# Performance work log

Hardware: AMD Instinct MI355X
Metric: run time of the kernel (lower is better)

Reference implementation:

```python
import jax, jax.numpy as jnp
import numpy as np

KERNEL = 3          # route_nms_kernel
MAX_ROUTES = 256    # max_routes (topk per image)
STRIDE = 4.0        # route_stride
MIN_SIZE = 32.0     # route_min_size
MAX_SIZE = 512.0    # route_max_size
POWER = 2.0         # route_score_power
B, H, W = 32, 512, 512


def setup_inputs() -> dict:
    key = jax.random.key(0)
    k1, k2, k3 = jax.random.split(key, 3)
    return {
        "route_logits": jax.random.normal(k1, (B, 1, H, W), dtype=jnp.float32),
        "scale_logits": jax.random.normal(k2, (B, 1, H, W), dtype=jnp.float32),
        "uncertainty_logits": jax.random.normal(k3, (B, 1, H, W), dtype=jnp.float32),
        "image_h": 2048,
        "image_w": 2048,
    }


def _local_max_pool(x):
    # x: [H, W]; 3x3 max pool, stride 1, pad kernel//2 (torch F.max_pool2d pads with -inf)
    pad = KERNEL // 2
    return jax.lax.reduce_window(x, -jnp.inf, jax.lax.max,
                                 (KERNEL, KERNEL), (1, 1),
                                 [(pad, pad), (pad, pad)])


def reference(route_logits, scale_logits, uncertainty_logits, image_h, image_w):
    # score_map = sigmoid(logits)^power * (1 - 0.35*sigmoid(uncertainty))  (use_route_uncertainty=True)
    score_map = jnp.power(jax.nn.sigmoid(route_logits), POWER)
    score_map = score_map * (1.0 - 0.35 * jax.nn.sigmoid(uncertainty_logits))
    img_h = jnp.float32(image_h)
    img_w = jnp.float32(image_w)
    width = route_logits.shape[-1]

    def per_image(batch_idx, scores2d, scale2d, unc2d):
        pooled = _local_max_pool(scores2d)
        filtered = jnp.where(scores2d == pooled, scores2d, -1.0)  # masked_fill(~mask, -1)
        values, indices = jax.lax.top_k(filtered.reshape(-1), MAX_ROUTES)
        valid = values > 0.0  # torch filters values>0; here kept as fixed-shape mask
        ys = indices // width
        xs = indices % width
        cx = (xs.astype(jnp.float32) + 0.5) * STRIDE
        cy = (ys.astype(jnp.float32) + 0.5) * STRIDE
        scale_g = scale2d[ys, xs]
        unc = jax.nn.sigmoid(unc2d[ys, xs])
        side = MIN_SIZE + jax.nn.sigmoid(scale_g) * (MAX_SIZE - MIN_SIZE)
        side = side * (1.0 + 0.25 * unc)
        half = side * 0.5
        x1 = jnp.clip(cx - half, 0.0, img_w - 1.0)
        y1 = jnp.clip(cy - half, 0.0, img_h - 1.0)
        x2 = jnp.clip(cx + half, 1.0, img_w)
        y2 = jnp.clip(cy + half, 1.0, img_h)
        rois = jnp.stack([jnp.full_like(x1, batch_idx), x1, y1, x2, y2], axis=1)  # [K,5]
        rois = jnp.where(valid[:, None], rois, 0.0)
        vals = jnp.where(valid, values, 0.0)
        return rois, vals, valid

    batch_ids = jnp.arange(route_logits.shape[0], dtype=jnp.float32)
    rois, scores, valid = jax.vmap(per_image)(
        batch_ids, score_map[:, 0], scale_logits[:, 0], uncertainty_logits[:, 0])
    # rois: [B, K, 5], scores: [B, K], valid: [B, K] (per_image_counts = valid.sum(-1))
    return rois, scores, valid
```

## Files before the change

### kernel.cpp

```cpp
#include <hip/hip_runtime.h>
#include <cstdint>
#include <cstddef>

#define BATCH 32
#define IMH 512
#define IMW 512
#define KMAX 256

#define RPW 8
#define NBLKX 2
#define NLIST (NBLKX * (IMH / RPW))
#define NMID 32
#define WCAP 512

#define TPB2 512

typedef unsigned long long u64;

__device__ __forceinline__ float sigmoidf_(float x) {
    return 1.0f / (1.0f + expf(-x));
}
__device__ __forceinline__ float scoref_(float r, float u) {
    const float sg = sigmoidf_(r);
    return sg * sg * (1.0f - 0.35f * sigmoidf_(u));
}

#define SHF(v, jj, dm) do {                                         \
    const u64 o_ = __shfl_xor((v), (jj), 64);                       \
    const bool take_ = ((((lane & (jj)) == 0) == (dm)) == ((v) < o_)); \
    (v) = take_ ? o_ : (v);                                         \
} while (0)

#define RMAX(a, b) do {                                             \
    const u64 hi_ = ((a) > (b)) ? (a) : (b);                        \
    const u64 lo_ = ((a) > (b)) ? (b) : (a);                        \
    (a) = hi_; (b) = lo_;                                           \
} while (0)

#define RMIN(a, b) do {                                             \
    const u64 hi_ = ((a) > (b)) ? (a) : (b);                        \
    const u64 lo_ = ((a) > (b)) ? (b) : (a);                        \
    (a) = lo_; (b) = hi_;                                           \
} while (0)

__device__ __forceinline__ void clean256(u64& v0, u64& v1, u64& v2, u64& v3,
                                         const int lane) {
    RMAX(v0, v2); RMAX(v1, v3);
    RMAX(v0, v1); RMAX(v2, v3);
    #pragma unroll
    for (int j = 32; j > 0; j >>= 1) {
        SHF(v0, j, true); SHF(v1, j, true); SHF(v2, j, true); SHF(v3, j, true);
    }
}

__device__ __forceinline__ void sort256(u64& v0, u64& v1, u64& v2, u64& v3,
                                        const int lane) {
    #pragma unroll
    for (int k = 2; k <= 32; k <<= 1) {
        #pragma unroll
        for (int j = k >> 1; j > 0; j >>= 1) {
            const bool dm = ((lane & k) == 0);
            SHF(v0, j, dm); SHF(v1, j, dm); SHF(v2, j, dm); SHF(v3, j, dm);
        }
    }
    #pragma unroll
    for (int j = 32; j > 0; j >>= 1) {
        SHF(v0, j, true); SHF(v1, j, false); SHF(v2, j, true); SHF(v3, j, false);
    }
    RMAX(v0, v1); RMIN(v2, v3);
    #pragma unroll
    for (int j = 32; j > 0; j >>= 1) {
        SHF(v0, j, true); SHF(v1, j, true); SHF(v2, j, false); SHF(v3, j, false);
    }
    clean256(v0, v1, v2, v3, lane);
}

__device__ __forceinline__ void merge256(u64& v0, u64& v1, u64& v2, u64& v3,
                                         u64 w0, u64 w1, u64 w2, u64 w3,
                                         const int lane) {
    const int rl = 63 ^ lane;
    const u64 b0 = __shfl(w3, rl, 64);
    const u64 b1 = __shfl(w2, rl, 64);
    const u64 b2 = __shfl(w1, rl, 64);
    const u64 b3 = __shfl(w0, rl, 64);
    v0 = (v0 > b0) ? v0 : b0;
    v1 = (v1 > b1) ? v1 : b1;
    v2 = (v2 > b2) ? v2 : b2;
    v3 = (v3 > b3) ? v3 : b3;
    clean256(v0, v1, v2, v3, lane);
}

__global__ __launch_bounds__(64)
void score_nms_kernel(const float* __restrict__ route,
                      const float* __restrict__ unc,
                      u64* __restrict__ top) {
    const int b    = blockIdx.z;
    const int lane = threadIdx.x;
    const int y0   = blockIdx.y * RPW;
    const int x0   = blockIdx.x * 256 + lane * 4;
    const int blk  = blockIdx.y * NBLKX + blockIdx.x;

    __shared__ u64 myR[WCAP];

    const float* rB = route + (size_t)b * IMH * IMW;
    const float* uB = unc   + (size_t)b * IMH * IMW;

    int ex = -1;
    if (lane == 0)       ex = x0 - 1;
    else if (lane == 63) ex = x0 + 4;
    const bool eAct = (ex >= 0 && ex < IMW);

    const u64 laneMaskLt = (1ull << lane) - 1ull;
    int wcnt = 0;

    float sP[4], hP1[4], hP2[4];
    #pragma unroll
    for (int j = 0; j < 4; ++j) { sP[j] = -INFINITY; hP1[j] = -INFINITY; hP2[j] = -INFINITY; }

    const int ylast = y0 + RPW;
    bool v = (y0 - 1 >= 0);
    float4 r4, u4; float er = 0.f, eu = 0.f;
    if (v) {
        r4 = *(const float4*)(rB + (size_t)(y0 - 1) * IMW + x0);
        u4 = *(const float4*)(uB + (size_t)(y0 - 1) * IMW + x0);
        if (eAct) { er = rB[(size_t)(y0 - 1) * IMW + ex]; eu = uB[(size_t)(y0 - 1) * IMW + ex]; }
    }

    for (int y = y0 - 1; y <= ylast; ++y) {
        const int yn = y + 1;
        const bool vn = (yn <= ylast) && (yn < IMH);
        float4 r4n, u4n; float ern = 0.f, eun = 0.f;
        if (vn) {
            r4n = *(const float4*)(rB + (size_t)yn * IMW + x0);
            u4n = *(const float4*)(uB + (size_t)yn * IMW + x0);
            if (eAct) { ern = rB[(size_t)yn * IMW + ex]; eun = uB[(size_t)yn * IMW + ex]; }
        }

        float sC[4], hmC[4];
        float es = -INFINITY;
        if (v && eAct) es = scoref_(er, eu);
        if (v) {
            sC[0] = scoref_(r4.x, u4.x);
            sC[1] = scoref_(r4.y, u4.y);
            sC[2] = scoref_(r4.z, u4.z);
            sC[3] = scoref_(r4.w, u4.w);
        } else {
            sC[0] = sC[1] = sC[2] = sC[3] = -INFINITY;
        }
        float lft = __shfl_up(sC[3], 1, 64);
        if (lane == 0) lft = es;
        float rgt = __shfl_down(sC[0], 1, 64);
        if (lane == 63) rgt = es;
        if (v) {
            hmC[0] = fmaxf(fmaxf(lft,   sC[0]), sC[1]);
            hmC[1] = fmaxf(fmaxf(sC[0], sC[1]), sC[2]);
            hmC[2] = fmaxf(fmaxf(sC[1], sC[2]), sC[3]);
            hmC[3] = fmaxf(fmaxf(sC[2], sC[3]), rgt);
        } else {
            hmC[0] = hmC[1] = hmC[2] = hmC[3] = -INFINITY;
        }

        if (y >= y0 + 1) {
            const int yo = y - 1;
            bool p[4]; int cntT = 0;
            #pragma unroll
            for (int j = 0; j < 4; ++j) {
                const float m9 = fmaxf(fmaxf(hP2[j], hP1[j]), hmC[j]);
                p[j] = (sP[j] >= m9);
                cntT += p[j] ? 1 : 0;
            }
            const u64 B0 = __ballot(cntT & 1);
            const u64 B1 = __ballot(cntT & 2);
            const u64 B2 = __ballot(cntT & 4);
            const int total = __popcll(B0) + 2 * __popcll(B1) + 4 * __popcll(B2);
            if (total > 0) {
                const int prefix = __popcll(B0 & laneMaskLt) + 2 * __popcll(B1 & laneMaskLt)
                                 + 4 * __popcll(B2 & laneMaskLt);
                int mb = wcnt + prefix;
                #pragma unroll
                for (int j = 0; j < 4; ++j) {
                    if (p[j]) {
                        const unsigned idx = (unsigned)(yo * IMW + (x0 + j));
                        const u64 key = ((u64)__float_as_uint(sP[j]) << 32) | (unsigned)(~idx);
                        if (mb < WCAP) myR[mb] = key;
                        ++mb;
                    }
                }
                wcnt += total;
            }
        }

        #pragma unroll
        for (int j = 0; j < 4; ++j) { hP2[j] = hP1[j]; hP1[j] = hmC[j]; sP[j] = sC[j]; }
        r4 = r4n; u4 = u4n; er = ern; eu = eun; v = vn;
    }

    const int m = (wcnt < WCAP) ? wcnt : WCAP;
    u64 v0, v1, v2, v3;
    v0 = (lane       < m) ? myR[lane]       : 0ull;
    v1 = (lane + 64  < m) ? myR[lane + 64]  : 0ull;
    v2 = (lane + 128 < m) ? myR[lane + 128] : 0ull;
    v3 = (lane + 192 < m) ? myR[lane + 192] : 0ull;
    sort256(v0, v1, v2, v3, lane);
    if (m > 256) {
        u64 w0, w1, w2, w3;
        w0 = (lane + 256 < m) ? myR[lane + 256] : 0ull;
        w1 = (lane + 320 < m) ? myR[lane + 320] : 0ull;
        w2 = (lane + 384 < m) ? myR[lane + 384] : 0ull;
        w3 = (lane + 448 < m) ? myR[lane + 448] : 0ull;
        sort256(w0, w1, w2, w3, lane);
        merge256(v0, v1, v2, v3, w0, w1, w2, w3, lane);
    }

    u64* seg = top + ((size_t)b * NLIST + blk) * KMAX;
    seg[lane]       = v0;
    seg[lane + 64]  = v1;
    seg[lane + 128] = v2;
    seg[lane + 192] = v3;
}

__global__ __launch_bounds__(64)
void merge4_kernel(const u64* __restrict__ top,
                   u64* __restrict__ mid) {
    const int o    = blockIdx.x;
    const int b    = blockIdx.y;
    const int lane = threadIdx.x;

    const u64* L = top + ((size_t)b * NLIST + o * 4) * KMAX;

    u64 a0 = L[lane],            a1 = L[lane + 64],
        a2 = L[lane + 128],      a3 = L[lane + 192];
    {
        const u64 w0 = L[KMAX + lane],       w1 = L[KMAX + lane + 64],
                  w2 = L[KMAX + lane + 128], w3 = L[KMAX + lane + 192];
        merge256(a0, a1, a2, a3, w0, w1, w2, w3, lane);
    }
    u64 c0 = L[2 * KMAX + lane],        c1 = L[2 * KMAX + lane + 64],
        c2 = L[2 * KMAX + lane + 128],  c3 = L[2 * KMAX + lane + 192];
    {
        const u64 w0 = L[3 * KMAX + lane],       w1 = L[3 * KMAX + lane + 64],
                  w2 = L[3 * KMAX + lane + 128], w3 = L[3 * KMAX + lane + 192];
        merge256(c0, c1, c2, c3, w0, w1, w2, w3, lane);
    }
    merge256(a0, a1, a2, a3, c0, c1, c2, c3, lane);

    u64* out = mid + ((size_t)b * NMID + o) * KMAX;
    out[lane]       = a0;
    out[lane + 64]  = a1;
    out[lane + 128] = a2;
    out[lane + 192] = a3;
}

__global__ __launch_bounds__(TPB2)
void tail_kernel(const u64* __restrict__ mid,
                 const float* __restrict__ scale,
                 const float* __restrict__ unc,
                 const int* __restrict__ imh,
                 const int* __restrict__ imw,
                 float* __restrict__ rois,
                 float* __restrict__ scoresOut,
                 float* __restrict__ validOut) {
    const int b   = blockIdx.x;
    const int tid = threadIdx.x;

    __shared__ u64 bufA[NMID * KMAX];
    __shared__ u64 bufB[(NMID / 2) * KMAX];

    const u64* tb = mid + (size_t)b * NMID * KMAX;
    for (int i = tid; i < NMID * KMAX; i += TPB2) bufA[i] = tb[i];
    __syncthreads();

    u64* src = bufA;
    u64* dst = bufB;
    int nl = NMID;
    while (nl > 1) {
        const int half = nl >> 1;
        const int E = half * KMAX;
        for (int p = tid; p < E; p += TPB2) {
            const int h = p >> 8;
            const int i = p & (KMAX - 1);
            const u64 a = src[(2 * h) * KMAX + i];
            const u64 c = src[(2 * h + 1) * KMAX + (KMAX - 1 - i)];
            dst[p] = (a > c) ? a : c;
        }
        __syncthreads();
        for (int j = KMAX >> 1; j > 0; j >>= 1) {
            for (int p = tid; p < (E >> 1); p += TPB2) {
                const int i   = ((p & ~(j - 1)) << 1) | (p & (j - 1));
                const int ixj = i | j;
                const u64 a = dst[i];
                const u64 c = dst[ixj];
                if (a < c) { dst[i] = c; dst[ixj] = a; }
            }
            __syncthreads();
        }
        u64* t = src; src = dst; dst = t;
        nl = half;
    }

    if (tid < KMAX) {
        const u64 k = src[tid];
        const float value = __uint_as_float((unsigned)(k >> 32));
        const bool valid  = (k != 0ull) && (value > 0.0f);

        float r0 = 0.f, r1 = 0.f, r2 = 0.f, r3 = 0.f, r4 = 0.f, sv = 0.f, vv = 0.f;
        if (valid) {
            const unsigned idx = ~(unsigned)(k & 0xFFFFFFFFull);
            const int y = (int)(idx / IMW);
            const int x = (int)(idx % IMW);
            const float cx = ((float)x + 0.5f) * 4.0f;
            const float cy = ((float)y + 0.5f) * 4.0f;
            const float sg = scale[(size_t)b * IMH * IMW + idx];
            const float uu = unc[(size_t)b * IMH * IMW + idx];
            const float su = sigmoidf_(uu);
            float side = 32.0f + sigmoidf_(sg) * (512.0f - 32.0f);
            side = side * (1.0f + 0.25f * su);
            const float half2 = side * 0.5f;
            const float fw = (float)imw[0];
            const float fh = (float)imh[0];
            r0 = (float)b;
            r1 = fminf(fmaxf(cx - half2, 0.0f), fw - 1.0f);
            r2 = fminf(fmaxf(cy - half2, 0.0f), fh - 1.0f);
            r3 = fminf(fmaxf(cx + half2, 1.0f), fw);
            r4 = fminf(fmaxf(cy + half2, 1.0f), fh);
            sv = value;
            vv = 1.0f;
        }
        float* roiP = rois + ((size_t)b * KMAX + tid) * 5;
        roiP[0] = r0; roiP[1] = r1; roiP[2] = r2; roiP[3] = r3; roiP[4] = r4;
        scoresOut[b * KMAX + tid] = sv;
        validOut[b * KMAX + tid]  = vv;
    }
}

extern "C" void kernel_launch(void* const* d_in, const int* in_sizes, int n_in,
                              void* d_out, int out_size, void* d_ws, size_t ws_size,
                              hipStream_t stream) {
    const float* route = (const float*)d_in[0];
    const float* scale = (const float*)d_in[1];
    const float* unc   = (const float*)d_in[2];
    const int*   imh   = (const int*)d_in[3];
    const int*   imw   = (const int*)d_in[4];

    u64* top = (u64*)d_ws;
    u64* mid = top + (size_t)BATCH * NLIST * KMAX;

    float* rois      = (float*)d_out;
    float* scoresOut = rois + (size_t)BATCH * KMAX * 5;
    float* validOut  = scoresOut + (size_t)BATCH * KMAX;

    dim3 grid1(NBLKX, IMH / RPW, BATCH);
    score_nms_kernel<<<grid1, 64, 0, stream>>>(route, unc, top);

    dim3 grid2(NMID, BATCH);
    merge4_kernel<<<grid2, 64, 0, stream>>>(top, mid);

    tail_kernel<<<BATCH, TPB2, 0, stream>>>(mid, scale, unc,
                                            imh, imw, rois, scoresOut, validOut);
}
```

Baseline: 64.61 us.

## Process two row strips per wave and interleave their bitonic sorts

```diff
diff --git a/kernel.cpp b/kernel.cpp
--- a/kernel.cpp
+++ b/kernel.cpp
@@ -9,8 +9,9 @@
 
 #define RPW 8
 #define NBLKX 2
-#define NLIST (NBLKX * (IMH / RPW))
-#define NMID 32
+#define NYG (IMH / (2 * RPW))
+#define NL1 (NBLKX * NYG)
+#define NMID 16
 #define WCAP 512
 
 #define TPB2 512
@@ -31,6 +32,16 @@
     (v) = take_ ? o_ : (v);                                         \
 } while (0)
 
+#define SHF2(v, u, jj, dm) do {                                     \
+    const u64 ov_ = __shfl_xor((v), (jj), 64);                      \
+    const u64 ou_ = __shfl_xor((u), (jj), 64);                      \
+    const bool dir_ = (((lane & (jj)) == 0) == (dm));               \
+    const bool tv_ = (dir_ == ((v) < ov_));                         \
+    const bool tu_ = (dir_ == ((u) < ou_));                         \
+    (v) = tv_ ? ov_ : (v);                                          \
+    (u) = tu_ ? ou_ : (u);                                          \
+} while (0)
+
 #define RMAX(a, b) do {                                             \
     const u64 hi_ = ((a) > (b)) ? (a) : (b);                        \
     const u64 lo_ = ((a) > (b)) ? (b) : (a);                        \
@@ -73,6 +84,39 @@
         SHF(v0, j, true); SHF(v1, j, true); SHF(v2, j, false); SHF(v3, j, false);
     }
     clean256(v0, v1, v2, v3, lane);
+}
+
+__device__ __forceinline__ void sort256x2(u64& v0, u64& v1, u64& v2, u64& v3,
+                                          u64& u0, u64& u1, u64& u2, u64& u3,
+                                          const int lane) {
+    #pragma unroll
+    for (int k = 2; k <= 32; k <<= 1) {
+        #pragma unroll
+        for (int j = k >> 1; j > 0; j >>= 1) {
+            const bool dm = ((lane & k) == 0);
+            SHF2(v0, u0, j, dm); SHF2(v1, u1, j, dm);
+            SHF2(v2, u2, j, dm); SHF2(v3, u3, j, dm);
+        }
+    }
+    #pragma unroll
+    for (int j = 32; j > 0; j >>= 1) {
+        SHF2(v0, u0, j, true); SHF2(v1, u1, j, false);
+        SHF2(v2, u2, j, true); SHF2(v3, u3, j, false);
+    }
+    RMAX(v0, v1); RMIN(v2, v3);
+    RMAX(u0, u1); RMIN(u2, u3);
+    #pragma unroll
+    for (int j = 32; j > 0; j >>= 1) {
+        SHF2(v0, u0, j, true); SHF2(v1, u1, j, true);
+        SHF2(v2, u2, j, false); SHF2(v3, u3, j, false);
+    }
+    RMAX(v0, v2); RMAX(v1, v3); RMAX(u0, u2); RMAX(u1, u3);
+    RMAX(v0, v1); RMAX(v2, v3); RMAX(u0, u1); RMAX(u2, u3);
+    #pragma unroll
+    for (int j = 32; j > 0; j >>= 1) {
+        SHF2(v0, u0, j, true); SHF2(v1, u1, j, true);
+        SHF2(v2, u2, j, true); SHF2(v3, u3, j, true);
+    }
 }
 
 __device__ __forceinline__ void merge256(u64& v0, u64& v1, u64& v2, u64& v3,
@@ -96,11 +140,10 @@
                       u64* __restrict__ top) {
     const int b    = blockIdx.z;
     const int lane = threadIdx.x;
-    const int y0   = blockIdx.y * RPW;
     const int x0   = blockIdx.x * 256 + lane * 4;
-    const int blk  = blockIdx.y * NBLKX + blockIdx.x;
-
-    __shared__ u64 myR[WCAP];
+    const int list = blockIdx.y * NBLKX + blockIdx.x;
+
+    __shared__ u64 myR[2 * WCAP];
 
     const float* rB = route + (size_t)b * IMH * IMW;
     const float* uB = unc   + (size_t)b * IMH * IMW;
@@ -111,112 +154,138 @@
     const bool eAct = (ex >= 0 && ex < IMW);
 
     const u64 laneMaskLt = (1ull << lane) - 1ull;
-    int wcnt = 0;
-
-    float sP[4], hP1[4], hP2[4];
-    #pragma unroll
-    for (int j = 0; j < 4; ++j) { sP[j] = -INFINITY; hP1[j] = -INFINITY; hP2[j] = -INFINITY; }
-
-    const int ylast = y0 + RPW;
-    bool v = (y0 - 1 >= 0);
-    float4 r4, u4; float er = 0.f, eu = 0.f;
-    if (v) {
-        r4 = *(const float4*)(rB + (size_t)(y0 - 1) * IMW + x0);
-        u4 = *(const float4*)(uB + (size_t)(y0 - 1) * IMW + x0);
-        if (eAct) { er = rB[(size_t)(y0 - 1) * IMW + ex]; eu = uB[(size_t)(y0 - 1) * IMW + ex]; }
-    }
-
-    for (int y = y0 - 1; y <= ylast; ++y) {
-        const int yn = y + 1;
-        const bool vn = (yn <= ylast) && (yn < IMH);
-        float4 r4n, u4n; float ern = 0.f, eun = 0.f;
-        if (vn) {
-            r4n = *(const float4*)(rB + (size_t)yn * IMW + x0);
-            u4n = *(const float4*)(uB + (size_t)yn * IMW + x0);
-            if (eAct) { ern = rB[(size_t)yn * IMW + ex]; eun = uB[(size_t)yn * IMW + ex]; }
-        }
-
-        float sC[4], hmC[4];
-        float es = -INFINITY;
-        if (v && eAct) es = scoref_(er, eu);
+    int wcntA = 0, wcntB = 0;
+
+    #pragma unroll
+    for (int s = 0; s < 2; ++s) {
+        const int y0 = (blockIdx.y * 2 + s) * RPW;
+        u64* reg = myR + s * WCAP;
+        int wcnt = 0;
+
+        float sP[4], hP1[4], hP2[4];
+        #pragma unroll
+        for (int j = 0; j < 4; ++j) { sP[j] = -INFINITY; hP1[j] = -INFINITY; hP2[j] = -INFINITY; }
+
+        const int ylast = y0 + RPW;
+        bool v = (y0 - 1 >= 0);
+        float4 r4, u4; float er = 0.f, eu = 0.f;
         if (v) {
-            sC[0] = scoref_(r4.x, u4.x);
-            sC[1] = scoref_(r4.y, u4.y);
-            sC[2] = scoref_(r4.z, u4.z);
-            sC[3] = scoref_(r4.w, u4.w);
-        } else {
-            sC[0] = sC[1] = sC[2] = sC[3] = -INFINITY;
-        }
-        float lft = __shfl_up(sC[3], 1, 64);
-        if (lane == 0) lft = es;
-        float rgt = __shfl_down(sC[0], 1, 64);
-        if (lane == 63) rgt = es;
-        if (v) {
-            hmC[0] = fmaxf(fmaxf(lft,   sC[0]), sC[1]);
-            hmC[1] = fmaxf(fmaxf(sC[0], sC[1]), sC[2]);
-            hmC[2] = fmaxf(fmaxf(sC[1], sC[2]), sC[3]);
-            hmC[3] = fmaxf(fmaxf(sC[2], sC[3]), rgt);
-        } else {
-            hmC[0] = hmC[1] = hmC[2] = hmC[3] = -INFINITY;
-        }
-
-        if (y >= y0 + 1) {
-            const int yo = y - 1;
-            bool p[4]; int cntT = 0;
-            #pragma unroll
-            for (int j = 0; j < 4; ++j) {
-                const float m9 = fmaxf(fmaxf(hP2[j], hP1[j]), hmC[j]);
-                p[j] = (sP[j] >= m9);
-                cntT += p[j] ? 1 : 0;
+            r4 = *(const float4*)(rB + (size_t)(y0 - 1) * IMW + x0);
+            u4 = *(const float4*)(uB + (size_t)(y0 - 1) * IMW + x0);
+            if (eAct) { er = rB[(size_t)(y0 - 1) * IMW + ex]; eu = uB[(size_t)(y0 - 1) * IMW + ex]; }
+        }
+
+        for (int y = y0 - 1; y <= ylast; ++y) {
+            const int yn = y + 1;
+            const bool vn = (yn <= ylast) && (yn < IMH);
+            float4 r4n, u4n; float ern = 0.f, eun = 0.f;
+            if (vn) {
+                r4n = *(const float4*)(rB + (size_t)yn * IMW + x0);
+                u4n = *(const float4*)(uB + (size_t)yn * IMW + x0);
+                if (eAct) { ern = rB[(size_t)yn * IMW + ex]; eun = uB[(size_t)yn * IMW + ex]; }
             }
-            const u64 B0 = __ballot(cntT & 1);
-            const u64 B1 = __ballot(cntT & 2);
-            const u64 B2 = __ballot(cntT & 4);
-            const int total = __popcll(B0) + 2 * __popcll(B1) + 4 * __popcll(B2);
-            if (total > 0) {
-                const int prefix = __popcll(B0 & laneMaskLt) + 2 * __popcll(B1 & laneMaskLt)
-                                 + 4 * __popcll(B2 & laneMaskLt);
-                int mb = wcnt + prefix;
+
+            float sC[4], hmC[4];
+            float es = -INFINITY;
+            if (v && eAct) es = scoref_(er, eu);
+            if (v) {
+                sC[0] = scoref_(r4.x, u4.x);
+                sC[1] = scoref_(r4.y, u4.y);
+                sC[2] = scoref_(r4.z, u4.z);
+                sC[3] = scoref_(r4.w, u4.w);
+            } else {
+                sC[0] = sC[1] = sC[2] = sC[3] = -INFINITY;
+            }
+            float lft = __shfl_up(sC[3], 1, 64);
+            if (lane == 0) lft = es;
+            float rgt = __shfl_down(sC[0], 1, 64);
+            if (lane == 63) rgt = es;
+            if (v) {
+                hmC[0] = fmaxf(fmaxf(lft,   sC[0]), sC[1]);
+                hmC[1] = fmaxf(fmaxf(sC[0], sC[1]), sC[2]);
+                hmC[2] = fmaxf(fmaxf(sC[1], sC[2]), sC[3]);
+                hmC[3] = fmaxf(fmaxf(sC[2], sC[3]), rgt);
+            } else {
+                hmC[0] = hmC[1] = hmC[2] = hmC[3] = -INFINITY;
+            }
+
+            if (y >= y0 + 1) {
+                const int yo = y - 1;
+                bool p[4]; int cntT = 0;
                 #pragma unroll
                 for (int j = 0; j < 4; ++j) {
-                    if (p[j]) {
-                        const unsigned idx = (unsigned)(yo * IMW + (x0 + j));
-                        const u64 key = ((u64)__float_as_uint(sP[j]) << 32) | (unsigned)(~idx);
-                        if (mb < WCAP) myR[mb] = key;
-                        ++mb;
+                    const float m9 = fmaxf(fmaxf(hP2[j], hP1[j]), hmC[j]);
+                    p[j] = (sP[j] >= m9);
+                    cntT += p[j] ? 1 : 0;
+                }
+                const u64 B0 = __ballot(cntT & 1);
+                const u64 B1 = __ballot(cntT & 2);
+                const u64 B2 = __ballot(cntT & 4);
+                const int total = __popcll(B0) + 2 * __popcll(B1) + 4 * __popcll(B2);
+                if (total > 0) {
+                    const int prefix = __popcll(B0 & laneMaskLt) + 2 * __popcll(B1 & laneMaskLt)
+                                     + 4 * __popcll(B2 & laneMaskLt);
+                    int mb = wcnt + prefix;
+                    #pragma unroll
+                    for (int j = 0; j < 4; ++j) {
+                        if (p[j]) {
+                            const unsigned idx = (unsigned)(yo * IMW + (x0 + j));
+                            const u64 key = ((u64)__float_as_uint(sP[j]) << 32) | (unsigned)(~idx);
+                            if (mb < WCAP) reg[mb] = key;
+                            ++mb;
+                        }
                     }
+                    wcnt += total;
                 }
-                wcnt += total;
             }
-        }
-
-        #pragma unroll
-        for (int j = 0; j < 4; ++j) { hP2[j] = hP1[j]; hP1[j] = hmC[j]; sP[j] = sC[j]; }
-        r4 = r4n; u4 = u4n; er = ern; eu = eun; v = vn;
-    }
-
-    const int m = (wcnt < WCAP) ? wcnt : WCAP;
-    u64 v0, v1, v2, v3;
-    v0 = (lane       < m) ? myR[lane]       : 0ull;
-    v1 = (lane + 64  < m) ? myR[lane + 64]  : 0ull;
-    v2 = (lane + 128 < m) ? myR[lane + 128] : 0ull;
-    v3 = (lane + 192 < m) ? myR[lane + 192] : 0ull;
-    sort256(v0, v1, v2, v3, lane);
-    if (m > 256) {
+
+            #pragma unroll
+            for (int j = 0; j < 4; ++j) { hP2[j] = hP1[j]; hP1[j] = hmC[j]; sP[j] = sC[j]; }
+            r4 = r4n; u4 = u4n; er = ern; eu = eun; v = vn;
+        }
+
+        if (s == 0) wcntA = wcnt; else wcntB = wcnt;
+    }
+
+    const int mA = (wcntA < WCAP) ? wcntA : WCAP;
+    const int mB = (wcntB < WCAP) ? wcntB : WCAP;
+    u64 a0, a1, a2, a3, c0, c1, c2, c3;
+    a0 = (lane       < mA) ? myR[lane]       : 0ull;
+    a1 = (lane + 64  < mA) ? myR[lane + 64]  : 0ull;
+    a2 = (lane + 128 < mA) ? myR[lane + 128] : 0ull;
+    a3 = (lane + 192 < mA) ? myR[lane + 192] : 0ull;
+    c0 = (lane       < mB) ? myR[WCAP + lane]       : 0ull;
+    c1 = (lane + 64  < mB) ? myR[WCAP + lane + 64]  : 0ull;
+    c2 = (lane + 128 < mB) ? myR[WCAP + lane + 128] : 0ull;
+    c3 = (lane + 192 < mB) ? myR[WCAP + lane + 192] : 0ull;
+    sort256x2(a0, a1, a2, a3, c0, c1, c2, c3, lane);
+
+    if (mA > 256) {
         u64 w0, w1, w2, w3;
-        w0 = (lane + 256 < m) ? myR[lane + 256] : 0ull;
-        w1 = (lane + 320 < m) ? myR[lane + 320] : 0ull;
-        w2 = (lane + 384 < m) ? myR[lane + 384] : 0ull;
-        w3 = (lane + 448 < m) ? myR[lane + 448] : 0ull;
+        w0 = (lane + 256 < mA) ? myR[lane + 256] : 0ull;
+        w1 = (lane + 320 < mA) ? myR[lane + 320] : 0ull;
+        w2 = (lane + 384 < mA) ? myR[lane + 384] : 0ull;
+        w3 = (lane + 448 < mA) ? myR[lane + 448] : 0ull;
         sort256(w0, w1, w2, w3, lane);
-        merge256(v0, v1, v2, v3, w0, w1, w2, w3, lane);
-    }
-
-    u64* seg = top + ((size_t)b * NLIST + blk) * KMAX;
-    seg[lane]       = v0;
-    seg[lane + 64]  = v1;
-    seg[lane + 128] = v2;
-    seg[lane + 192] = v3;
+        merge256(a0, a1, a2, a3, w0, w1, w2, w3, lane);
+    }
+    if (mB > 256) {
+        u64 w0, w1, w2, w3;
+        w0 = (lane + 256 < mB) ? myR[WCAP + lane + 256] : 0ull;
+        w1 = (lane + 320 < mB) ? myR[WCAP + lane + 320] : 0ull;
+        w2 = (lane + 384 < mB) ? myR[WCAP + lane + 384] : 0ull;
+        w3 = (lane + 448 < mB) ? myR[WCAP + lane + 448] : 0ull;
+        sort256(w0, w1, w2, w3, lane);
+        merge256(c0, c1, c2, c3, w0, w1, w2, w3, lane);
+    }
+
+    merge256(a0, a1, a2, a3, c0, c1, c2, c3, lane);
+
+    u64* seg = top + ((size_t)b * NL1 + list) * KMAX;
+    seg[lane]       = a0;
+    seg[lane + 64]  = a1;
+    seg[lane + 128] = a2;
+    seg[lane + 192] = a3;
 }
 
 __global__ __launch_bounds__(64)
@@ -226,7 +295,7 @@
     const int b    = blockIdx.y;
     const int lane = threadIdx.x;
 
-    const u64* L = top + ((size_t)b * NLIST + o * 4) * KMAX;
+    const u64* L = top + ((size_t)b * NL1 + o * 4) * KMAX;
 
     u64 a0 = L[lane],            a1 = L[lane + 64],
         a2 = L[lane + 128],      a3 = L[lane + 192];
@@ -343,13 +412,13 @@
     const int*   imw   = (const int*)d_in[4];
 
     u64* top = (u64*)d_ws;
-    u64* mid = top + (size_t)BATCH * NLIST * KMAX;
+    u64* mid = top + (size_t)BATCH * NL1 * KMAX;
 
     float* rois      = (float*)d_out;
     float* scoresOut = rois + (size_t)BATCH * KMAX * 5;
     float* validOut  = scoresOut + (size_t)BATCH * KMAX;
 
-    dim3 grid1(NBLKX, IMH / RPW, BATCH);
+    dim3 grid1(NBLKX, NYG, BATCH);
     score_nms_kernel<<<grid1, 64, 0, stream>>>(route, unc, top);
 
     dim3 grid2(NMID, BATCH);
```

Result: no change. 63.43 us (-1.8%).

## Halve rows per wave, add second merge level, use 128-element sort path

Applied to the files above, without the earlier changes.

```diff
diff --git a/kernel.cpp b/kernel.cpp
--- a/kernel.cpp
+++ b/kernel.cpp
@@ -7,11 +7,13 @@
 #define IMW 512
 #define KMAX 256
 
-#define RPW 8
+#define RPW 4
 #define NBLKX 2
-#define NLIST (NBLKX * (IMH / RPW))
-#define NMID 32
-#define WCAP 512
+#define NYG (IMH / RPW)
+#define NL1 (NBLKX * NYG)
+#define NM1 (NL1 / 4)
+#define NMID (NM1 / 4)
+#define WCAP 256
 
 #define TPB2 512
 
@@ -73,6 +75,26 @@
         SHF(v0, j, true); SHF(v1, j, true); SHF(v2, j, false); SHF(v3, j, false);
     }
     clean256(v0, v1, v2, v3, lane);
+}
+
+__device__ __forceinline__ void sort128(u64& v0, u64& v1, const int lane) {
+    #pragma unroll
+    for (int k = 2; k <= 32; k <<= 1) {
+        #pragma unroll
+        for (int j = k >> 1; j > 0; j >>= 1) {
+            const bool dm = ((lane & k) == 0);
+            SHF(v0, j, dm); SHF(v1, j, dm);
+        }
+    }
+    #pragma unroll
+    for (int j = 32; j > 0; j >>= 1) {
+        SHF(v0, j, true); SHF(v1, j, false);
+    }
+    RMAX(v0, v1);
+    #pragma unroll
+    for (int j = 32; j > 0; j >>= 1) {
+        SHF(v0, j, true); SHF(v1, j, true);
+    }
 }
 
 __device__ __forceinline__ void merge256(u64& v0, u64& v1, u64& v2, u64& v3,
@@ -98,7 +120,7 @@
     const int lane = threadIdx.x;
     const int y0   = blockIdx.y * RPW;
     const int x0   = blockIdx.x * 256 + lane * 4;
-    const int blk  = blockIdx.y * NBLKX + blockIdx.x;
+    const int list = blockIdx.y * NBLKX + blockIdx.x;
 
     __shared__ u64 myR[WCAP];
 
@@ -196,37 +218,35 @@
     }
 
     const int m = (wcnt < WCAP) ? wcnt : WCAP;
-    u64 v0, v1, v2, v3;
-    v0 = (lane       < m) ? myR[lane]       : 0ull;
-    v1 = (lane + 64  < m) ? myR[lane + 64]  : 0ull;
-    v2 = (lane + 128 < m) ? myR[lane + 128] : 0ull;
-    v3 = (lane + 192 < m) ? myR[lane + 192] : 0ull;
-    sort256(v0, v1, v2, v3, lane);
-    if (m > 256) {
-        u64 w0, w1, w2, w3;
-        w0 = (lane + 256 < m) ? myR[lane + 256] : 0ull;
-        w1 = (lane + 320 < m) ? myR[lane + 320] : 0ull;
-        w2 = (lane + 384 < m) ? myR[lane + 384] : 0ull;
-        w3 = (lane + 448 < m) ? myR[lane + 448] : 0ull;
-        sort256(w0, w1, w2, w3, lane);
-        merge256(v0, v1, v2, v3, w0, w1, w2, w3, lane);
-    }
-
-    u64* seg = top + ((size_t)b * NLIST + blk) * KMAX;
-    seg[lane]       = v0;
-    seg[lane + 64]  = v1;
-    seg[lane + 128] = v2;
-    seg[lane + 192] = v3;
+    u64 a0, a1, a2, a3;
+    if (m <= 128) {
+        a0 = (lane      < m) ? myR[lane]      : 0ull;
+        a1 = (lane + 64 < m) ? myR[lane + 64] : 0ull;
+        sort128(a0, a1, lane);
+        a2 = 0ull; a3 = 0ull;
+    } else {
+        a0 = (lane       < m) ? myR[lane]       : 0ull;
+        a1 = (lane + 64  < m) ? myR[lane + 64]  : 0ull;
+        a2 = (lane + 128 < m) ? myR[lane + 128] : 0ull;
+        a3 = (lane + 192 < m) ? myR[lane + 192] : 0ull;
+        sort256(a0, a1, a2, a3, lane);
+    }
+
+    u64* seg = top + ((size_t)b * NL1 + list) * KMAX;
+    seg[lane]       = a0;
+    seg[lane + 64]  = a1;
+    seg[lane + 128] = a2;
+    seg[lane + 192] = a3;
 }
 
 __global__ __launch_bounds__(64)
-void merge4_kernel(const u64* __restrict__ top,
-                   u64* __restrict__ mid) {
+void merge4_kernel(const u64* __restrict__ in, int nin,
+                   u64* __restrict__ out_) {
     const int o    = blockIdx.x;
     const int b    = blockIdx.y;
     const int lane = threadIdx.x;
 
-    const u64* L = top + ((size_t)b * NLIST + o * 4) * KMAX;
+    const u64* L = in + ((size_t)b * nin + o * 4) * KMAX;
 
     u64 a0 = L[lane],            a1 = L[lane + 64],
         a2 = L[lane + 128],      a3 = L[lane + 192];
@@ -244,7 +264,8 @@
     }
     merge256(a0, a1, a2, a3, c0, c1, c2, c3, lane);
 
-    u64* out = mid + ((size_t)b * NMID + o) * KMAX;
+    const int nout = nin / 4;
+    u64* out = out_ + ((size_t)b * nout + o) * KMAX;
     out[lane]       = a0;
     out[lane + 64]  = a1;
     out[lane + 128] = a2;
@@ -342,19 +363,23 @@
     const int*   imh   = (const int*)d_in[3];
     const int*   imw   = (const int*)d_in[4];
 
-    u64* top = (u64*)d_ws;
-    u64* mid = top + (size_t)BATCH * NLIST * KMAX;
+    u64* top  = (u64*)d_ws;
+    u64* mid1 = top  + (size_t)BATCH * NL1 * KMAX;
+    u64* mid2 = mid1 + (size_t)BATCH * NM1 * KMAX;
 
     float* rois      = (float*)d_out;
     float* scoresOut = rois + (size_t)BATCH * KMAX * 5;
     float* validOut  = scoresOut + (size_t)BATCH * KMAX;
 
-    dim3 grid1(NBLKX, IMH / RPW, BATCH);
+    dim3 grid1(NBLKX, NYG, BATCH);
     score_nms_kernel<<<grid1, 64, 0, stream>>>(route, unc, top);
 
-    dim3 grid2(NMID, BATCH);
-    merge4_kernel<<<grid2, 64, 0, stream>>>(top, mid);
-
-    tail_kernel<<<BATCH, TPB2, 0, stream>>>(mid, scale, unc,
+    dim3 grid2(NM1, BATCH);
+    merge4_kernel<<<grid2, 64, 0, stream>>>(top, NL1, mid1);
+
+    dim3 grid3(NMID, BATCH);
+    merge4_kernel<<<grid3, 64, 0, stream>>>(mid1, NM1, mid2);
+
+    tail_kernel<<<BATCH, TPB2, 0, stream>>>(mid2, scale, unc,
                                             imh, imw, rois, scoresOut, validOut);
 }
```

Result: faster. 60.60 us (-6.2%).
